# Kernel tuning notes

Measured on AMD Instinct MI355X. Metric: run time of the kernel, lower is better.

Reference implementation:

```python
import jax, jax.numpy as jnp
import numpy as np

B, C, L = 32, 128, 256  # batch, channels (graph nodes), temporal features (= feas)
K = 2  # Chebyshev order (hardcoded in the module)


def setup_inputs() -> dict:
    key = jax.random.key(0)
    k1, k2, k3 = jax.random.split(key, 3)
    x = jax.random.normal(k1, (B, C, L), dtype=jnp.float32)
    a = jax.random.uniform(k2, (C, C), dtype=jnp.float32)  # nn.Parameter(torch.rand)
    Theta = jax.random.normal(k3, (K, L, L), dtype=jnp.float32)  # (k, feas, num_of_filters)
    return {"x": x, "a": a, "Theta": Theta}


def reference(x, a, Theta):
    b, c, l = x.shape
    # pairwise L1 distance over the feature axis: diff[b,i,j] = sum_l |x[b,i,l] - x[b,j,l]|
    diff = jnp.abs(x[:, :, None, :] - x[:, None, :, :]).sum(-1)  # [b,c,c]
    # F.normalize(diff, dim=0): L2-normalize across the batch dimension
    norm = jnp.sqrt((diff * diff).sum(axis=0, keepdims=True))
    diff = diff / jnp.maximum(norm, 1e-12)
    # learned adjacency
    tmpS = jnp.exp(jax.nn.relu((1.0 - diff) * a))        # [b,c,c]
    adj = tmpS / tmpS.sum(axis=1, keepdims=True)
    deg = adj.sum(axis=1)                                 # [b,c]
    I = jnp.eye(c, dtype=x.dtype)
    D = deg[:, :, None] * I                               # diag_embed(deg)
    Lap = D - adj
    lambda_max = 2.0
    L_t = 2.0 * Lap / lambda_max - I                      # scaled Laplacian, [b,c,c]
    cheb = [jnp.broadcast_to(I, (b, c, c)), L_t]
    for i in range(2, K):
        cheb.append(2.0 * L_t * cheb[i - 1] - cheb[i - 2])
    out = jnp.zeros((b, c, Theta.shape[2]), dtype=x.dtype)
    for kk in range(K):
        # rhs = bmm(T_k^T, x): rhs[b,j,l] = sum_i T_k[b,i,j] * x[b,i,l]
        rhs = jnp.einsum('bij,bil->bjl', cheb[kk], x)
        out = out + rhs @ Theta[kk]
    return jax.nn.relu(out)
```

## Files before the change

### kernel.cpp

```cpp
#include <hip/hip_runtime.h>
#include <hip/hip_bf16.h>


#define NB 32
#define NC 128
#define NL 256

typedef short bf16x8 __attribute__((ext_vector_type(8)));
typedef float f32x4 __attribute__((ext_vector_type(4)));

static __device__ __forceinline__ unsigned short f2bf(float f) {
    unsigned u = __builtin_bit_cast(unsigned, f);
    u += 0x7fff + ((u >> 16) & 1);
    return (unsigned short)(u >> 16);
}

__global__ __launch_bounds__(256) void k_cvt(const float* __restrict__ x,
                                             const float* __restrict__ Theta,
                                             unsigned short* __restrict__ xb,
                                             unsigned short* __restrict__ thT) {
    int idx = blockIdx.x * 256 + threadIdx.x;
    if (idx < 262144) {
        float4 v = ((const float4*)x)[idx];
        ushort4 o;
        o.x = f2bf(v.x); o.y = f2bf(v.y); o.z = f2bf(v.z); o.w = f2bf(v.w);
        ((ushort4*)xb)[idx] = o;
    } else {
        int e = idx - 262144;
        int t = e >> 16, n = (e >> 8) & 255, l = e & 255;
        thT[e] = f2bf(Theta[t * 65536 + l * 256 + n]);
    }
}

__device__ const unsigned char TI36[36] = {0,0,0,0,0,0,0,0, 1,1,1,1,1,1,1, 2,2,2,2,2,2,
                                           3,3,3,3,3, 4,4,4,4, 5,5,5, 6,6, 7};
__device__ const unsigned char TJ36[36] = {0,1,2,3,4,5,6,7, 1,2,3,4,5,6,7, 2,3,4,5,6,7,
                                           3,4,5,6,7, 4,5,6,7, 5,6,7, 6,7, 7};

__global__ __launch_bounds__(256) void k_pairdist(const float* __restrict__ x,
                                                  float* __restrict__ diff) {
    int bid = blockIdx.x;
    int b = bid / 36, p = bid - b * 36;
    int i0 = TI36[p] * 16, j0 = TJ36[p] * 16;
    __shared__ float xi[16 * 260];
    __shared__ float xj[16 * 260];
    __shared__ float sT[16 * 17];
    const float4* x4 = (const float4*)(x + (size_t)b * NC * NL);
    int tid = threadIdx.x;
    for (int idx = tid; idx < 16 * 64; idx += 256) {
        int r = idx >> 6, c = idx & 63;
        *(float4*)&xi[r * 260 + c * 4] = x4[(i0 + r) * 64 + c];
        *(float4*)&xj[r * 260 + c * 4] = x4[(j0 + r) * 64 + c];
    }
    __syncthreads();
    int il = tid >> 4, jl = tid & 15;
    float acc = 0.f;
    #pragma unroll 8
    for (int l4 = 0; l4 < 64; ++l4) {
        float4 u = *(const float4*)&xi[il * 260 + l4 * 4];
        float4 v = *(const float4*)&xj[jl * 260 + l4 * 4];
        acc += fabsf(u.x - v.x) + fabsf(u.y - v.y) +
               fabsf(u.z - v.z) + fabsf(u.w - v.w);
    }
    float* D = diff + (size_t)b * NC * NC;
    D[(i0 + il) * NC + j0 + jl] = acc;
    sT[jl * 17 + il] = acc;
    __syncthreads();
    D[(j0 + il) * NC + i0 + jl] = sT[il * 17 + jl];
}

__global__ __launch_bounds__(256) void k_norm_at(const float* __restrict__ diff,
                                                 const float* __restrict__ a,
                                                 float* __restrict__ rnorm,
                                                 float* __restrict__ aT) {
    int idx = blockIdx.x * 256 + threadIdx.x;
    float s = 0.f;
    #pragma unroll
    for (int b = 0; b < NB; ++b) {
        float v = diff[(size_t)b * NC * NC + idx];
        s = fmaf(v, v, s);
    }
    rnorm[idx] = 1.0f / fmaxf(sqrtf(s), 1e-12f);
    int i = idx >> 7, j = idx & 127;
    aT[j * NC + i] = a[idx];
}

__global__ __launch_bounds__(128) void k_adjt(const float* __restrict__ diff,
                                              const float* __restrict__ rnorm,
                                              const float* __restrict__ aT,
                                              unsigned short* __restrict__ adjTb) {
    int bid = blockIdx.x;
    int b = bid >> 7, j = bid & 127;
    int i = threadIdx.x;
    float d  = diff[(size_t)b * NC * NC + j * NC + i];
    float rn = rnorm[j * NC + i];
    float av = aT[j * NC + i];
    float s = expf(fmaxf((1.0f - d * rn) * av, 0.0f));
    float t = s;
    #pragma unroll
    for (int off = 32; off; off >>= 1) t += __shfl_xor(t, off);
    __shared__ float partial[2];
    if ((threadIdx.x & 63) == 0) partial[threadIdx.x >> 6] = t;
    __syncthreads();
    float total = partial[0] + partial[1];
    adjTb[(size_t)b * NC * NC + j * NC + i] = f2bf(s / total);
}

__global__ __launch_bounds__(256) void k_gemm_xth(const unsigned short* __restrict__ xb,
                                                  const unsigned short* __restrict__ thT,
                                                  float* __restrict__ xTh0,
                                                  unsigned short* __restrict__ xTh1T) {
    int bid = blockIdx.x;
    int mt = bid >> 4, nt = bid & 15;
    int m0 = mt * 64, n0 = nt * 32;
    int tid = threadIdx.x, w = tid >> 6, lane = tid & 63;
    int lr = lane & 15, lg = lane >> 4;
    const unsigned short* Ap  = xb  + (size_t)(m0 + w * 16 + lr) * 256 + lg * 8;
    const unsigned short* Bp0 = thT + (size_t)(n0 + lr) * 256 + lg * 8;
    const unsigned short* Bp1 = Bp0 + 16 * 256;
    f32x4 acc0 = {0.f, 0.f, 0.f, 0.f}, acc1 = {0.f, 0.f, 0.f, 0.f};
    #pragma unroll
    for (int ks = 0; ks < 8; ++ks) {
        bf16x8 av = *(const bf16x8*)(Ap + ks * 32);
        bf16x8 b0 = *(const bf16x8*)(Bp0 + ks * 32);
        bf16x8 b1 = *(const bf16x8*)(Bp1 + ks * 32);
        acc0 = __builtin_amdgcn_mfma_f32_16x16x32_bf16(av, b0, acc0, 0, 0, 0);
        acc1 = __builtin_amdgcn_mfma_f32_16x16x32_bf16(av, b1, acc1, 0, 0, 0);
    }
    int orow = m0 + w * 16 + lg * 4;
    int bt = orow >> 7, ir = orow & 127;
    if (n0 < 256) {
        float* O = xTh0 + (size_t)bt * 32768 + (size_t)ir * 256 + n0 + lr;
        #pragma unroll
        for (int r = 0; r < 4; ++r) {
            O[r * 256]      = acc0[r];
            O[r * 256 + 16] = acc1[r];
        }
    } else {
        int n1 = n0 - 256;
        unsigned short* O = xTh1T + (size_t)bt * 32768 + (size_t)(n1 + lr) * 128 + ir;
        ushort4 p0, p1;
        p0.x = f2bf(acc0[0]); p0.y = f2bf(acc0[1]); p0.z = f2bf(acc0[2]); p0.w = f2bf(acc0[3]);
        p1.x = f2bf(acc1[0]); p1.y = f2bf(acc1[1]); p1.z = f2bf(acc1[2]); p1.w = f2bf(acc1[3]);
        *(ushort4*)O = p0;
        *(ushort4*)(O + 16 * 128) = p1;
    }
}

__global__ __launch_bounds__(256) void k_gemm_e(const unsigned short* __restrict__ adjTb,
                                                const unsigned short* __restrict__ xTh1T,
                                                const float* __restrict__ xTh0,
                                                float* __restrict__ out) {
    int bid = blockIdx.x;
    int b = bid >> 4, t16 = bid & 15;
    int j0 = (t16 >> 3) * 64, n0 = (t16 & 7) * 32;
    int tid = threadIdx.x, w = tid >> 6, lane = tid & 63;
    int lr = lane & 15, lg = lane >> 4;
    const unsigned short* Ap  = adjTb + (size_t)b * 16384 + (size_t)(j0 + w * 16 + lr) * 128 + lg * 8;
    const unsigned short* Bp0 = xTh1T + (size_t)b * 32768 + (size_t)(n0 + lr) * 128 + lg * 8;
    const unsigned short* Bp1 = Bp0 + 16 * 128;
    f32x4 acc0 = {0.f, 0.f, 0.f, 0.f}, acc1 = {0.f, 0.f, 0.f, 0.f};
    #pragma unroll
    for (int ks = 0; ks < 4; ++ks) {
        bf16x8 av = *(const bf16x8*)(Ap + ks * 32);
        bf16x8 b0 = *(const bf16x8*)(Bp0 + ks * 32);
        bf16x8 b1 = *(const bf16x8*)(Bp1 + ks * 32);
        acc0 = __builtin_amdgcn_mfma_f32_16x16x32_bf16(av, b0, acc0, 0, 0, 0);
        acc1 = __builtin_amdgcn_mfma_f32_16x16x32_bf16(av, b1, acc1, 0, 0, 0);
    }
    int j = j0 + w * 16 + lg * 4;
    const float* X0 = xTh0 + (size_t)b * 32768 + (size_t)j * 256 + n0 + lr;
    float* O = out + (size_t)b * 32768 + (size_t)j * 256 + n0 + lr;
    #pragma unroll
    for (int r = 0; r < 4; ++r) {
        O[r * 256]      = fmaxf(X0[r * 256]      - acc0[r], 0.f);
        O[r * 256 + 16] = fmaxf(X0[r * 256 + 16] - acc1[r], 0.f);
    }
}

extern "C" void kernel_launch(void* const* d_in, const int* in_sizes, int n_in,
                              void* d_out, int out_size, void* d_ws, size_t ws_size,
                              hipStream_t stream) {
    const float* x     = (const float*)d_in[0];
    const float* a     = (const float*)d_in[1];
    const float* Theta = (const float*)d_in[2];
    float* out = (float*)d_out;
    float* f0  = (float*)d_ws;

    float*          diff  = f0;
    unsigned short* xTh1T = (unsigned short*)f0;
    float*          rnorm = f0 + 524288;
    float*          aT    = f0 + 540672;
    float*          xTh0  = f0 + 557056;
    unsigned short* xb    = (unsigned short*)(f0 + 1605632);
    unsigned short* thT   = (unsigned short*)(f0 + 2129920);
    unsigned short* adjTb = (unsigned short*)(f0 + 2195456);

    k_cvt     <<<dim3(1536), dim3(256), 0, stream>>>(x, Theta, xb, thT);
    k_pairdist<<<dim3(NB * 36), dim3(256), 0, stream>>>(x, diff);
    k_norm_at <<<dim3(64), dim3(256), 0, stream>>>(diff, a, rnorm, aT);
    k_adjt    <<<dim3(NB * NC), dim3(128), 0, stream>>>(diff, rnorm, aT, adjTb);
    k_gemm_xth<<<dim3(1024), dim3(256), 0, stream>>>(xb, thT, xTh0, xTh1T);
    k_gemm_e  <<<dim3(512), dim3(256), 0, stream>>>(adjTb, xTh1T, xTh0, out);
}
```

Before: 100.3 us.

## Merge preprocessing kernels, fold norm into adjacency, retile x·Theta GEMM with LDS

Combines the bf16 conversion, pairwise-distance, Theta transpose and a-transpose work into one heterogeneous launch, and drops the separate norm kernel by having each adjacency block recompute the batch-wise L2 norm itself. Theta is now transposed through shared memory instead of with strided scalar reads. The x·Theta GEMM doubles its M tile to 128 and stages the B tile in swizzled LDS so each wave computes a 32x32 output. The aim is fewer launches and less redundant global traffic, at the cost of 32x redundant norm reads per (i,j) in the adjacency kernel and a fast-math exp.

```diff
diff --git a/kernel.cpp b/kernel.cpp
--- a/kernel.cpp
+++ b/kernel.cpp
@@ -15,142 +15,179 @@
     return (unsigned short)(u >> 16);
 }
 
-__global__ __launch_bounds__(256) void k_cvt(const float* __restrict__ x,
+__device__ const unsigned char TI36[36] = {0,0,0,0,0,0,0,0, 1,1,1,1,1,1,1, 2,2,2,2,2,2,
+                                           3,3,3,3,3, 4,4,4,4, 5,5,5, 6,6, 7};
+__device__ const unsigned char TJ36[36] = {0,1,2,3,4,5,6,7, 1,2,3,4,5,6,7, 2,3,4,5,6,7,
+                                           3,4,5,6,7, 4,5,6,7, 5,6,7, 6,7, 7};
+
+__global__ __launch_bounds__(256) void k_pre(const float* __restrict__ x,
                                              const float* __restrict__ Theta,
+                                             const float* __restrict__ a,
+                                             float* __restrict__ diff,
                                              unsigned short* __restrict__ xb,
-                                             unsigned short* __restrict__ thT) {
-    int idx = blockIdx.x * 256 + threadIdx.x;
-    if (idx < 262144) {
+                                             unsigned short* __restrict__ thT,
+                                             float* __restrict__ aT) {
+    __shared__ float smem[8592];
+    int bid = blockIdx.x;
+    int tid = threadIdx.x;
+
+    if (bid < 1152) {
+        int b = bid / 36, p = bid - b * 36;
+        int i0 = TI36[p] * 16, j0 = TJ36[p] * 16;
+        float* xi = smem;
+        float* xj = smem + 4160;
+        float* sT = smem + 8320;
+        const float4* x4 = (const float4*)(x + (size_t)b * NC * NL);
+        for (int idx = tid; idx < 16 * 64; idx += 256) {
+            int r = idx >> 6, c = idx & 63;
+            *(float4*)&xi[r * 260 + c * 4] = x4[(i0 + r) * 64 + c];
+            *(float4*)&xj[r * 260 + c * 4] = x4[(j0 + r) * 64 + c];
+        }
+        __syncthreads();
+        int il = tid >> 4, jl = tid & 15;
+        float acc = 0.f;
+        #pragma unroll 8
+        for (int l4 = 0; l4 < 64; ++l4) {
+            float4 u = *(const float4*)&xi[il * 260 + l4 * 4];
+            float4 v = *(const float4*)&xj[jl * 260 + l4 * 4];
+            acc += fabsf(u.x - v.x) + fabsf(u.y - v.y) +
+                   fabsf(u.z - v.z) + fabsf(u.w - v.w);
+        }
+        float* D = diff + (size_t)b * NC * NC;
+        D[(i0 + il) * NC + j0 + jl] = acc;
+        sT[jl * 17 + il] = acc;
+        __syncthreads();
+        D[(j0 + il) * NC + i0 + jl] = sT[il * 17 + jl];
+    } else if (bid < 2176) {
+        int idx = (bid - 1152) * 256 + tid;
         float4 v = ((const float4*)x)[idx];
         ushort4 o;
         o.x = f2bf(v.x); o.y = f2bf(v.y); o.z = f2bf(v.z); o.w = f2bf(v.w);
         ((ushort4*)xb)[idx] = o;
+    } else if (bid < 2208) {
+        int tt = bid - 2176;
+        int t = tt >> 4, rem = tt & 15;
+        int l0 = (rem >> 2) * 64, n0 = (rem & 3) * 64;
+        const float* Tp = Theta + (size_t)t * 65536;
+        for (int it = tid; it < 4096; it += 256) {
+            int r = it >> 6, c = it & 63;
+            smem[r * 65 + c] = Tp[(l0 + r) * 256 + n0 + c];
+        }
+        __syncthreads();
+        for (int it = tid; it < 4096; it += 256) {
+            int r = it >> 6, c = it & 63;
+            thT[(size_t)(t * 256 + n0 + r) * 256 + l0 + c] = f2bf(smem[c * 65 + r]);
+        }
     } else {
-        int e = idx - 262144;
-        int t = e >> 16, n = (e >> 8) & 255, l = e & 255;
-        thT[e] = f2bf(Theta[t * 65536 + l * 256 + n]);
-    }
-}
-
-__device__ const unsigned char TI36[36] = {0,0,0,0,0,0,0,0, 1,1,1,1,1,1,1, 2,2,2,2,2,2,
-                                           3,3,3,3,3, 4,4,4,4, 5,5,5, 6,6, 7};
-__device__ const unsigned char TJ36[36] = {0,1,2,3,4,5,6,7, 1,2,3,4,5,6,7, 2,3,4,5,6,7,
-                                           3,4,5,6,7, 4,5,6,7, 5,6,7, 6,7, 7};
-
-__global__ __launch_bounds__(256) void k_pairdist(const float* __restrict__ x,
-                                                  float* __restrict__ diff) {
-    int bid = blockIdx.x;
-    int b = bid / 36, p = bid - b * 36;
-    int i0 = TI36[p] * 16, j0 = TJ36[p] * 16;
-    __shared__ float xi[16 * 260];
-    __shared__ float xj[16 * 260];
-    __shared__ float sT[16 * 17];
-    const float4* x4 = (const float4*)(x + (size_t)b * NC * NL);
-    int tid = threadIdx.x;
-    for (int idx = tid; idx < 16 * 64; idx += 256) {
-        int r = idx >> 6, c = idx & 63;
-        *(float4*)&xi[r * 260 + c * 4] = x4[(i0 + r) * 64 + c];
-        *(float4*)&xj[r * 260 + c * 4] = x4[(j0 + r) * 64 + c];
-    }
-    __syncthreads();
-    int il = tid >> 4, jl = tid & 15;
-    float acc = 0.f;
-    #pragma unroll 8
-    for (int l4 = 0; l4 < 64; ++l4) {
-        float4 u = *(const float4*)&xi[il * 260 + l4 * 4];
-        float4 v = *(const float4*)&xj[jl * 260 + l4 * 4];
-        acc += fabsf(u.x - v.x) + fabsf(u.y - v.y) +
-               fabsf(u.z - v.z) + fabsf(u.w - v.w);
-    }
-    float* D = diff + (size_t)b * NC * NC;
-    D[(i0 + il) * NC + j0 + jl] = acc;
-    sT[jl * 17 + il] = acc;
-    __syncthreads();
-    D[(j0 + il) * NC + i0 + jl] = sT[il * 17 + jl];
-}
-
-__global__ __launch_bounds__(256) void k_norm_at(const float* __restrict__ diff,
-                                                 const float* __restrict__ a,
-                                                 float* __restrict__ rnorm,
-                                                 float* __restrict__ aT) {
-    int idx = blockIdx.x * 256 + threadIdx.x;
-    float s = 0.f;
-    #pragma unroll
-    for (int b = 0; b < NB; ++b) {
-        float v = diff[(size_t)b * NC * NC + idx];
-        s = fmaf(v, v, s);
-    }
-    rnorm[idx] = 1.0f / fmaxf(sqrtf(s), 1e-12f);
-    int i = idx >> 7, j = idx & 127;
-    aT[j * NC + i] = a[idx];
-}
-
-__global__ __launch_bounds__(128) void k_adjt(const float* __restrict__ diff,
-                                              const float* __restrict__ rnorm,
-                                              const float* __restrict__ aT,
-                                              unsigned short* __restrict__ adjTb) {
+        int tt = bid - 2208;
+        int i0 = (tt >> 1) * 64, j0 = (tt & 1) * 64;
+        for (int it = tid; it < 4096; it += 256) {
+            int r = it >> 6, c = it & 63;
+            smem[r * 65 + c] = a[(i0 + r) * NC + j0 + c];
+        }
+        __syncthreads();
+        for (int it = tid; it < 4096; it += 256) {
+            int r = it >> 6, c = it & 63;
+            aT[(j0 + r) * NC + i0 + c] = smem[c * 65 + r];
+        }
+    }
+}
+
+__global__ __launch_bounds__(128) void k_adj(const float* __restrict__ diff,
+                                             const float* __restrict__ aT,
+                                             unsigned short* __restrict__ adjTb) {
     int bid = blockIdx.x;
     int b = bid >> 7, j = bid & 127;
     int i = threadIdx.x;
-    float d  = diff[(size_t)b * NC * NC + j * NC + i];
-    float rn = rnorm[j * NC + i];
+    const float* Dj = diff + j * NC + i;
+    float ss = 0.f;
+    #pragma unroll
+    for (int bb = 0; bb < NB; ++bb) {
+        float v = Dj[(size_t)bb * NC * NC];
+        ss = fmaf(v, v, ss);
+    }
+    float rn = 1.0f / fmaxf(sqrtf(ss), 1e-12f);
+    float d  = Dj[(size_t)b * NC * NC];
     float av = aT[j * NC + i];
-    float s = expf(fmaxf((1.0f - d * rn) * av, 0.0f));
+    float s = __expf(fmaxf((1.0f - d * rn) * av, 0.0f));
     float t = s;
     #pragma unroll
     for (int off = 32; off; off >>= 1) t += __shfl_xor(t, off);
     __shared__ float partial[2];
-    if ((threadIdx.x & 63) == 0) partial[threadIdx.x >> 6] = t;
+    if ((i & 63) == 0) partial[i >> 6] = t;
     __syncthreads();
     float total = partial[0] + partial[1];
     adjTb[(size_t)b * NC * NC + j * NC + i] = f2bf(s / total);
 }
 
-__global__ __launch_bounds__(256) void k_gemm_xth(const unsigned short* __restrict__ xb,
-                                                  const unsigned short* __restrict__ thT,
-                                                  float* __restrict__ xTh0,
-                                                  unsigned short* __restrict__ xTh1T) {
+__global__ __launch_bounds__(256) void k_xth(const unsigned short* __restrict__ xb,
+                                             const unsigned short* __restrict__ thT,
+                                             float* __restrict__ xTh0,
+                                             unsigned short* __restrict__ xTh1T) {
+    __shared__ unsigned short Bs[8192];
     int bid = blockIdx.x;
     int mt = bid >> 4, nt = bid & 15;
-    int m0 = mt * 64, n0 = nt * 32;
+    int m0 = mt * 128, n0 = nt * 32;
     int tid = threadIdx.x, w = tid >> 6, lane = tid & 63;
     int lr = lane & 15, lg = lane >> 4;
-    const unsigned short* Ap  = xb  + (size_t)(m0 + w * 16 + lr) * 256 + lg * 8;
-    const unsigned short* Bp0 = thT + (size_t)(n0 + lr) * 256 + lg * 8;
-    const unsigned short* Bp1 = Bp0 + 16 * 256;
-    f32x4 acc0 = {0.f, 0.f, 0.f, 0.f}, acc1 = {0.f, 0.f, 0.f, 0.f};
+
+    #pragma unroll
+    for (int it = 0; it < 4; ++it) {
+        int c = tid + it * 256;
+        int n = c >> 5, kc = c & 31;
+        bf16x8 v = *(const bf16x8*)(thT + (size_t)(n0 + n) * 256 + kc * 8);
+        int dst = n * 512 + ((kc * 16) ^ ((n & 7) << 4));
+        *(bf16x8*)((char*)Bs + dst) = v;
+    }
+    __syncthreads();
+
+    const unsigned short* Ap0 = xb + (size_t)(m0 + w * 32 + lr) * 256 + lg * 8;
+    const unsigned short* Ap1 = Ap0 + 16 * 256;
+    f32x4 acc00 = {0.f,0.f,0.f,0.f}, acc01 = {0.f,0.f,0.f,0.f};
+    f32x4 acc10 = {0.f,0.f,0.f,0.f}, acc11 = {0.f,0.f,0.f,0.f};
+    int swz = (lr & 7) << 4;
     #pragma unroll
     for (int ks = 0; ks < 8; ++ks) {
-        bf16x8 av = *(const bf16x8*)(Ap + ks * 32);
-        bf16x8 b0 = *(const bf16x8*)(Bp0 + ks * 32);
-        bf16x8 b1 = *(const bf16x8*)(Bp1 + ks * 32);
-        acc0 = __builtin_amdgcn_mfma_f32_16x16x32_bf16(av, b0, acc0, 0, 0, 0);
-        acc1 = __builtin_amdgcn_mfma_f32_16x16x32_bf16(av, b1, acc1, 0, 0, 0);
-    }
-    int orow = m0 + w * 16 + lg * 4;
-    int bt = orow >> 7, ir = orow & 127;
+        bf16x8 a0 = *(const bf16x8*)(Ap0 + ks * 32);
+        bf16x8 a1 = *(const bf16x8*)(Ap1 + ks * 32);
+        int kb = (ks * 64 + lg * 16) ^ swz;
+        bf16x8 b0 = *(const bf16x8*)((char*)Bs + lr * 512 + kb);
+        bf16x8 b1 = *(const bf16x8*)((char*)Bs + (16 + lr) * 512 + kb);
+        acc00 = __builtin_amdgcn_mfma_f32_16x16x32_bf16(a0, b0, acc00, 0, 0, 0);
+        acc01 = __builtin_amdgcn_mfma_f32_16x16x32_bf16(a0, b1, acc01, 0, 0, 0);
+        acc10 = __builtin_amdgcn_mfma_f32_16x16x32_bf16(a1, b0, acc10, 0, 0, 0);
+        acc11 = __builtin_amdgcn_mfma_f32_16x16x32_bf16(a1, b1, acc11, 0, 0, 0);
+    }
+
+    int ir0 = w * 32 + lg * 4;
     if (n0 < 256) {
-        float* O = xTh0 + (size_t)bt * 32768 + (size_t)ir * 256 + n0 + lr;
+        float* O = xTh0 + (size_t)mt * 32768 + (size_t)ir0 * 256 + n0 + lr;
         #pragma unroll
         for (int r = 0; r < 4; ++r) {
-            O[r * 256]      = acc0[r];
-            O[r * 256 + 16] = acc1[r];
+            O[r * 256]              = acc00[r];
+            O[r * 256 + 16]         = acc01[r];
+            O[(16 + r) * 256]       = acc10[r];
+            O[(16 + r) * 256 + 16]  = acc11[r];
         }
     } else {
         int n1 = n0 - 256;
-        unsigned short* O = xTh1T + (size_t)bt * 32768 + (size_t)(n1 + lr) * 128 + ir;
-        ushort4 p0, p1;
-        p0.x = f2bf(acc0[0]); p0.y = f2bf(acc0[1]); p0.z = f2bf(acc0[2]); p0.w = f2bf(acc0[3]);
-        p1.x = f2bf(acc1[0]); p1.y = f2bf(acc1[1]); p1.z = f2bf(acc1[2]); p1.w = f2bf(acc1[3]);
-        *(ushort4*)O = p0;
-        *(ushort4*)(O + 16 * 128) = p1;
-    }
-}
-
-__global__ __launch_bounds__(256) void k_gemm_e(const unsigned short* __restrict__ adjTb,
-                                                const unsigned short* __restrict__ xTh1T,
-                                                const float* __restrict__ xTh0,
-                                                float* __restrict__ out) {
+        unsigned short* O = xTh1T + (size_t)mt * 32768;
+        ushort4 p;
+        p.x = f2bf(acc00[0]); p.y = f2bf(acc00[1]); p.z = f2bf(acc00[2]); p.w = f2bf(acc00[3]);
+        *(ushort4*)(O + (size_t)(n1 + lr) * 128 + ir0) = p;
+        p.x = f2bf(acc01[0]); p.y = f2bf(acc01[1]); p.z = f2bf(acc01[2]); p.w = f2bf(acc01[3]);
+        *(ushort4*)(O + (size_t)(n1 + 16 + lr) * 128 + ir0) = p;
+        p.x = f2bf(acc10[0]); p.y = f2bf(acc10[1]); p.z = f2bf(acc10[2]); p.w = f2bf(acc10[3]);
+        *(ushort4*)(O + (size_t)(n1 + lr) * 128 + ir0 + 16) = p;
+        p.x = f2bf(acc11[0]); p.y = f2bf(acc11[1]); p.z = f2bf(acc11[2]); p.w = f2bf(acc11[3]);
+        *(ushort4*)(O + (size_t)(n1 + 16 + lr) * 128 + ir0 + 16) = p;
+    }
+}
+
+__global__ __launch_bounds__(256) void k_out(const unsigned short* __restrict__ adjTb,
+                                             const unsigned short* __restrict__ xTh1T,
+                                             const float* __restrict__ xTh0,
+                                             float* __restrict__ out) {
     int bid = blockIdx.x;
     int b = bid >> 4, t16 = bid & 15;
     int j0 = (t16 >> 3) * 64, n0 = (t16 & 7) * 32;
@@ -159,7 +196,7 @@
     const unsigned short* Ap  = adjTb + (size_t)b * 16384 + (size_t)(j0 + w * 16 + lr) * 128 + lg * 8;
     const unsigned short* Bp0 = xTh1T + (size_t)b * 32768 + (size_t)(n0 + lr) * 128 + lg * 8;
     const unsigned short* Bp1 = Bp0 + 16 * 128;
-    f32x4 acc0 = {0.f, 0.f, 0.f, 0.f}, acc1 = {0.f, 0.f, 0.f, 0.f};
+    f32x4 acc0 = {0.f,0.f,0.f,0.f}, acc1 = {0.f,0.f,0.f,0.f};
     #pragma unroll
     for (int ks = 0; ks < 4; ++ks) {
         bf16x8 av = *(const bf16x8*)(Ap + ks * 32);
@@ -189,17 +226,14 @@
 
     float*          diff  = f0;
     unsigned short* xTh1T = (unsigned short*)f0;
-    float*          rnorm = f0 + 524288;
-    float*          aT    = f0 + 540672;
-    float*          xTh0  = f0 + 557056;
-    unsigned short* xb    = (unsigned short*)(f0 + 1605632);
-    unsigned short* thT   = (unsigned short*)(f0 + 2129920);
-    unsigned short* adjTb = (unsigned short*)(f0 + 2195456);
-
-    k_cvt     <<<dim3(1536), dim3(256), 0, stream>>>(x, Theta, xb, thT);
-    k_pairdist<<<dim3(NB * 36), dim3(256), 0, stream>>>(x, diff);
-    k_norm_at <<<dim3(64), dim3(256), 0, stream>>>(diff, a, rnorm, aT);
-    k_adjt    <<<dim3(NB * NC), dim3(128), 0, stream>>>(diff, rnorm, aT, adjTb);
-    k_gemm_xth<<<dim3(1024), dim3(256), 0, stream>>>(xb, thT, xTh0, xTh1T);
-    k_gemm_e  <<<dim3(512), dim3(256), 0, stream>>>(adjTb, xTh1T, xTh0, out);
-}
+    float*          aT    = f0 + 524288;
+    float*          xTh0  = f0 + 540672;
+    unsigned short* xb    = (unsigned short*)(f0 + 1589248);
+    unsigned short* thT   = (unsigned short*)(f0 + 2113536);
+    unsigned short* adjTb = (unsigned short*)(f0 + 2179072);
+
+    k_pre<<<dim3(2212), dim3(256), 0, stream>>>(x, Theta, a, diff, xb, thT, aT);
+    k_adj<<<dim3(NB * NC), dim3(128), 0, stream>>>(diff, aT, adjTb);
+    k_xth<<<dim3(512), dim3(256), 0, stream>>>(xb, thT, xTh0, xTh1T);
+    k_out<<<dim3(512), dim3(256), 0, stream>>>(adjTb, xTh1T, xTh0, out);
+}
```

Result: faster. 92.30 us (-8.0%).
